# Kernel optimization log

Hardware: AMD Instinct MI355X
Metric: run time of the kernel (lower is better)

Reference implementation:

```python
import jax, jax.numpy as jnp
import numpy as np

WS = 8      # window size
NH = 8      # num heads
DIM = 256
SHIFT = WS // 2  # shift=True path


def _relative_position_index(ws):
    coords = np.stack(np.meshgrid(np.arange(ws), np.arange(ws), indexing='ij'))  # [2,ws,ws]
    cf = coords.reshape(2, -1)
    rel = cf[:, :, None] - cf[:, None, :]            # [2,ws*ws,ws*ws]
    rel = rel.transpose(1, 2, 0)
    rel[:, :, 0] += ws - 1
    rel[:, :, 1] += ws - 1
    rel[:, :, 0] *= 2 * ws - 1
    return rel.sum(-1).astype(np.int32)              # [ws*ws,ws*ws]


def setup_inputs() -> dict:
    key = jax.random.key(0)
    ks = jax.random.split(key, 7)
    B, H, W, C = 2, 256, 256, DIM
    x = jax.random.normal(ks[0], (B, H, W, C), dtype=jnp.float32)
    qkv_w = jax.random.normal(ks[1], (3 * C, C), dtype=jnp.float32) * 0.02
    qkv_b = jnp.zeros((3 * C,), dtype=jnp.float32)
    proj_w = jax.random.normal(ks[2], (C, C), dtype=jnp.float32) * 0.02
    proj_b = jnp.zeros((C,), dtype=jnp.float32)
    bias_table = jax.random.normal(ks[3], ((2 * WS - 1) ** 2, NH), dtype=jnp.float32) * 0.02
    rel_index = jnp.asarray(_relative_position_index(WS))
    return {"x": x, "qkv_w": qkv_w, "qkv_b": qkv_b, "proj_w": proj_w,
            "proj_b": proj_b, "bias_table": bias_table, "rel_index": rel_index}


def reference(x, qkv_w, qkv_b, proj_w, proj_b, bias_table, rel_index):
    B, H, W, C = x.shape
    ws, nh = WS, NH
    hd = C // nh
    scale = hd ** -0.5
    n = ws * ws
    # cyclic shift
    x = jnp.roll(x, shift=(-SHIFT, -SHIFT), axis=(1, 2))
    # window partition -> [B*nW, ws*ws, C]
    xw = x.reshape(B, H // ws, ws, W // ws, ws, C)
    xw = xw.transpose(0, 1, 3, 2, 4, 5).reshape(-1, n, C)
    # qkv projection (torch Linear: y = x @ W.T + b)
    qkv = xw @ qkv_w.T + qkv_b
    qkv = qkv.reshape(-1, n, 3, nh, hd).transpose(2, 0, 3, 1, 4)  # [3, nW, nh, n, hd]
    q, k, v = qkv[0] * scale, qkv[1], qkv[2]
    attn = jnp.einsum('whid,whjd->whij', q, k)  # [nW, nh, n, n]
    bias = bias_table[rel_index.reshape(-1)].reshape(n, n, nh).transpose(2, 0, 1)
    attn = jax.nn.softmax(attn + bias[None], axis=-1)
    out = jnp.einsum('whij,whjd->whid', attn, v)               # [nW, nh, n, hd]
    out = out.transpose(0, 2, 1, 3).reshape(-1, n, C)
    out = out @ proj_w.T + proj_b
    # window reverse
    out = out.reshape(B, H // ws, W // ws, ws, ws, C)
    out = out.transpose(0, 1, 3, 2, 4, 5).reshape(B, H, W, C)
    return jnp.roll(out, shift=(SHIFT, SHIFT), axis=(1, 2))
```

## Files before the change

kernel.cpp:

```cpp
#include <hip/hip_runtime.h>
#include <hip/hip_bf16.h>

typedef _Float16 f16;
typedef _Float16 f16x8 __attribute__((ext_vector_type(8)));
typedef _Float16 f16x4 __attribute__((ext_vector_type(4)));
typedef float f32x4 __attribute__((ext_vector_type(4)));

#define SCALE 0.17677669529663687f

#define QW_OFF   0
#define PW_OFF   393216
#define QB_OFF   524288
#define BF_OFF   527360

__global__ __launch_bounds__(256) void prep_kernel(
    const float* __restrict__ qkv_w, const float* __restrict__ qkv_b,
    const float* __restrict__ proj_w, const float* __restrict__ bias_table,
    const int* __restrict__ rel_index,
    f16* __restrict__ qw_h, f16* __restrict__ pw_h,
    float* __restrict__ qb_s, float* __restrict__ bias_fr) {
  int i = blockIdx.x * 256 + threadIdx.x;
  if (i < 768 * 256) {
    float s = (i < 256 * 256) ? SCALE : 1.0f;
    qw_h[i] = (f16)(qkv_w[i] * s);
  }
  if (i < 768) qb_s[i] = qkv_b[i] * (i < 256 ? SCALE : 1.0f);
  if (i < 256 * 256) pw_h[i] = (f16)proj_w[i];
  if (i < 8 * 4 * 4 * 256) {
    int h = i >> 12, rest = i & 4095;
    int qt = rest >> 10, kt = (rest >> 8) & 3, l = (rest >> 2) & 63, r = i & 3;
    int q = qt * 16 + (l & 15);
    int ke = kt * 16 + 4 * (l >> 4) + r;
    bias_fr[i] = bias_table[rel_index[q * 64 + ke] * 8 + h];
  }
}

__global__ __launch_bounds__(256, 2) void fused_kernel(
    const float* __restrict__ x, const f16* __restrict__ qw_h,
    const float* __restrict__ qb_s, const float* __restrict__ bias_fr,
    const f16* __restrict__ pw_h, const float* __restrict__ proj_b,
    float* __restrict__ out) {

  __shared__ f16 sx[64 * 264];
  __shared__ f16 stg[4][5120];

  const int tid = threadIdx.x;
  const int lane = tid & 63;
  const int wv = tid >> 6;
  const int lo = lane & 15, hi = lane >> 4;

  const int win = blockIdx.x;
  const int b = win >> 10, wh = (win >> 5) & 31, ww = win & 31;

  {
    const int t = tid >> 2, q4 = tid & 3;
    const int r = t >> 3, c = t & 7;
    const int gr = (wh * 8 + r + 4) & 255;
    const int gc = (ww * 8 + c + 4) & 255;
    const float* src = x + (((size_t)(b * 256 + gr)) * 256 + gc) * 256;
#pragma unroll
    for (int i = 0; i < 8; ++i) {
      const int off = q4 * 8 + i * 32;
      float4 v0 = *(const float4*)(src + off);
      float4 v1 = *(const float4*)(src + off + 4);
      f16x8 hv;
      hv[0] = (f16)v0.x; hv[1] = (f16)v0.y; hv[2] = (f16)v0.z; hv[3] = (f16)v0.w;
      hv[4] = (f16)v1.x; hv[5] = (f16)v1.y; hv[6] = (f16)v1.z; hv[7] = (f16)v1.w;
      *(f16x8*)&sx[t * 264 + off] = hv;
    }
  }
  __syncthreads();

  f16* ws_ = &stg[wv][0];
  f16x8 qf[2][4];
  f16x8 kf[2][4];
  f16x8 vf[2][2][2];

#pragma unroll
  for (int bn = 0; bn < 3; ++bn) {
    const int fwave = bn * 256 + wv * 64;

    f32x4 acc[4][4];
#pragma unroll
    for (int nt = 0; nt < 4; ++nt)
#pragma unroll
      for (int mt = 0; mt < 4; ++mt) acc[nt][mt] = (f32x4){0.f, 0.f, 0.f, 0.f};

    f16x8 bf[2][4];
#pragma unroll
    for (int nt = 0; nt < 4; ++nt)
      bf[0][nt] = *(const f16x8*)&qw_h[(size_t)(fwave + nt * 16 + lo) * 256 + 8 * hi];

#pragma unroll
    for (int kt = 0; kt < 8; ++kt) {
      const int cur = kt & 1;
      if (kt < 7) {
#pragma unroll
        for (int nt = 0; nt < 4; ++nt)
          bf[cur ^ 1][nt] = *(const f16x8*)&qw_h[(size_t)(fwave + nt * 16 + lo) * 256 + (kt + 1) * 32 + 8 * hi];
      }
      f16x8 a[4];
#pragma unroll
      for (int mt = 0; mt < 4; ++mt)
        a[mt] = *(const f16x8*)&sx[(mt * 16 + lo) * 264 + kt * 32 + 8 * hi];
#pragma unroll
      for (int nt = 0; nt < 4; ++nt)
#pragma unroll
        for (int mt = 0; mt < 4; ++mt) {
          if (bn < 2)
            acc[nt][mt] = __builtin_amdgcn_mfma_f32_16x16x32_f16(bf[cur][nt], a[mt], acc[nt][mt], 0, 0, 0);
          else
            acc[nt][mt] = __builtin_amdgcn_mfma_f32_16x16x32_f16(a[mt], bf[cur][nt], acc[nt][mt], 0, 0, 0);
        }
    }

    if (bn < 2) {
#pragma unroll
      for (int nt = 0; nt < 4; ++nt) {
        const f32x4 bias4 = *(const f32x4*)&qb_s[fwave + nt * 16 + 4 * hi];
        const int base = (nt >> 1) * 2560 + (nt & 1) * 16 + 4 * hi;
#pragma unroll
        for (int mt = 0; mt < 4; ++mt) {
          f16x4 t;
#pragma unroll
          for (int r4 = 0; r4 < 4; ++r4) t[r4] = (f16)(acc[nt][mt][r4] + bias4[r4]);
          *(f16x4*)&ws_[base + (mt * 16 + lo) * 40] = t;
        }
      }
#pragma unroll
      for (int hsel = 0; hsel < 2; ++hsel)
#pragma unroll
        for (int t4 = 0; t4 < 4; ++t4) {
          f16x8 fr = *(const f16x8*)&ws_[hsel * 2560 + (t4 * 16 + lo) * 40 + 8 * hi];
          if (bn == 0) qf[hsel][t4] = fr; else kf[hsel][t4] = fr;
        }
    } else {
#pragma unroll
      for (int nt = 0; nt < 4; ++nt) {
        const float bias = qb_s[fwave + nt * 16 + lo];
        const int row = (nt >> 1) * 32 + (nt & 1) * 16 + lo;
#pragma unroll
        for (int mt = 0; mt < 4; ++mt) {
          f16x4 t;
#pragma unroll
          for (int r4 = 0; r4 < 4; ++r4) t[r4] = (f16)(acc[nt][mt][r4] + bias);
          *(f16x4*)&ws_[row * 72 + mt * 16 + 4 * hi] = t;
        }
      }
#pragma unroll
      for (int hsel = 0; hsel < 2; ++hsel)
#pragma unroll
        for (int kk = 0; kk < 2; ++kk)
#pragma unroll
          for (int dt = 0; dt < 2; ++dt)
            vf[hsel][kk][dt] = *(const f16x8*)&ws_[(hsel * 32 + dt * 16 + lo) * 72 + kk * 32 + 8 * hi];
    }
  }

  __syncthreads();
  f16* sao = sx;
  const f32x4 zero = {0.f, 0.f, 0.f, 0.f};
  f16x8 vone;
#pragma unroll
  for (int j = 0; j < 8; ++j) vone[j] = (f16)1.0f;

#pragma unroll
  for (int hsel = 0; hsel < 2; ++hsel) {
    const int h = 2 * wv + hsel;
#pragma unroll
    for (int qh = 0; qh < 2; ++qh) {
      f32x4 s[2][4];
#pragma unroll
      for (int q2 = 0; q2 < 2; ++q2)
#pragma unroll
        for (int kt = 0; kt < 4; ++kt)
          s[q2][kt] = *(const f32x4*)&bias_fr[(((h * 4 + qh * 2 + q2) * 4 + kt) << 8) + lane * 4];
#pragma unroll
      for (int q2 = 0; q2 < 2; ++q2)
#pragma unroll
        for (int kt = 0; kt < 4; ++kt)
          s[q2][kt] = __builtin_amdgcn_mfma_f32_16x16x32_f16(kf[hsel][kt], qf[hsel][qh * 2 + q2], s[q2][kt], 0, 0, 0);

#pragma unroll
      for (int q2 = 0; q2 < 2; ++q2)
#pragma unroll
        for (int kt = 0; kt < 4; ++kt) {
          f16x4 t;
#pragma unroll
          for (int r4 = 0; r4 < 4; ++r4) t[r4] = (f16)__expf(s[q2][kt][r4]);
          *(f16x4*)&ws_[(q2 * 16 + lo) * 72 + kt * 16 + 4 * hi] = t;
        }

      f32x4 o[2][2], oa[2];
#pragma unroll
      for (int q2 = 0; q2 < 2; ++q2) {
        oa[q2] = zero;
#pragma unroll
        for (int dt = 0; dt < 2; ++dt) o[q2][dt] = zero;
      }
#pragma unroll
      for (int kk = 0; kk < 2; ++kk) {
        f16x8 pB[2];
#pragma unroll
        for (int q2 = 0; q2 < 2; ++q2)
          pB[q2] = *(const f16x8*)&ws_[(q2 * 16 + lo) * 72 + kk * 32 + 8 * hi];
#pragma unroll
        for (int q2 = 0; q2 < 2; ++q2) {
          oa[q2] = __builtin_amdgcn_mfma_f32_16x16x32_f16(vone, pB[q2], oa[q2], 0, 0, 0);
#pragma unroll
          for (int dt = 0; dt < 2; ++dt)
            o[q2][dt] = __builtin_amdgcn_mfma_f32_16x16x32_f16(vf[hsel][kk][dt], pB[q2], o[q2][dt], 0, 0, 0);
        }
      }

#pragma unroll
      for (int q2 = 0; q2 < 2; ++q2) {
        const float inv = __builtin_amdgcn_rcpf(oa[q2][0]);
        const int tok = qh * 32 + q2 * 16 + lo;
#pragma unroll
        for (int dt = 0; dt < 2; ++dt) {
          f16x4 t;
#pragma unroll
          for (int r4 = 0; r4 < 4; ++r4) t[r4] = (f16)(o[q2][dt][r4] * inv);
          *(f16x4*)&sao[tok * 264 + h * 32 + dt * 16 + 4 * hi] = t;
        }
      }
    }
  }

  __syncthreads();

  f32x4 acc[4][4];
#pragma unroll
  for (int j = 0; j < 4; ++j)
#pragma unroll
    for (int mt = 0; mt < 4; ++mt) acc[j][mt] = (f32x4){0.f, 0.f, 0.f, 0.f};

#pragma unroll
  for (int kt = 0; kt < 8; ++kt) {
    f16x8 a[4];
#pragma unroll
    for (int mt = 0; mt < 4; ++mt)
      a[mt] = *(const f16x8*)&sao[(mt * 16 + lo) * 264 + kt * 32 + 8 * hi];
#pragma unroll
    for (int j = 0; j < 4; ++j) {
      const int n = (4 * wv + j) * 16 + lo;
      f16x8 bfp = *(const f16x8*)&pw_h[(size_t)n * 256 + kt * 32 + 8 * hi];
#pragma unroll
      for (int mt = 0; mt < 4; ++mt)
        acc[j][mt] = __builtin_amdgcn_mfma_f32_16x16x32_f16(a[mt], bfp, acc[j][mt], 0, 0, 0);
    }
  }

#pragma unroll
  for (int j = 0; j < 4; ++j) {
    const int n = (4 * wv + j) * 16 + lo;
    const float pb = proj_b[n];
#pragma unroll
    for (int mt = 0; mt < 4; ++mt)
#pragma unroll
      for (int r4 = 0; r4 < 4; ++r4) {
        const int token = mt * 16 + 4 * hi + r4;
        const int tr = token >> 3, tc = token & 7;
        const int gr = (wh * 8 + tr + 4) & 255;
        const int gc = (ww * 8 + tc + 4) & 255;
        out[(((size_t)(b * 256 + gr)) * 256 + gc) * 256 + n] = acc[j][mt][r4] + pb;
      }
  }
}

extern "C" void kernel_launch(void* const* d_in, const int* in_sizes, int n_in,
                              void* d_out, int out_size, void* d_ws, size_t ws_size,
                              hipStream_t stream) {
  const float* x          = (const float*)d_in[0];
  const float* qkv_w      = (const float*)d_in[1];
  const float* qkv_b      = (const float*)d_in[2];
  const float* proj_w     = (const float*)d_in[3];
  const float* proj_b     = (const float*)d_in[4];
  const float* bias_table = (const float*)d_in[5];
  const int*   rel_index  = (const int*)d_in[6];
  float* out = (float*)d_out;

  char* ws = (char*)d_ws;
  f16*   qw_h    = (f16*)(ws + QW_OFF);
  f16*   pw_h    = (f16*)(ws + PW_OFF);
  float* qb_s    = (float*)(ws + QB_OFF);
  float* bias_fr = (float*)(ws + BF_OFF);

  prep_kernel<<<768, 256, 0, stream>>>(qkv_w, qkv_b, proj_w, bias_table, rel_index,
                                       qw_h, pw_h, qb_s, bias_fr);
  fused_kernel<<<2048, 256, 0, stream>>>(x, qw_h, qb_s, bias_fr, pw_h, proj_b, out);
}
```

Measured before the change: 166.6 us.

## Shrink LDS with XOR swizzle, split QKV by head, prefetch proj weights

Replaces the padded 264-stride shared tile with an XOR-swizzled 256-stride layout and shrinks the per-wave staging buffer by processing the QKV projection one head (32 features) at a time. The smaller LDS footprint together with launch_bounds raised to 3 blocks per CU aims for higher occupancy. The output projection now double-buffers its weight fragments from global memory so loads can overlap the MFMAs. The trade-off is that the 3-block bound caps registers per thread, which may cause spills, and the QKV loop now runs as more, smaller passes.

```diff
diff --git a/kernel.cpp b/kernel.cpp
--- a/kernel.cpp
+++ b/kernel.cpp
@@ -12,6 +12,8 @@
 #define PW_OFF   393216
 #define QB_OFF   524288
 #define BF_OFF   527360
+
+#define SW(row, col) (((row) << 8) + ((col) ^ (((row) & 7) << 3)))
 
 __global__ __launch_bounds__(256) void prep_kernel(
     const float* __restrict__ qkv_w, const float* __restrict__ qkv_b,
@@ -35,14 +37,14 @@
   }
 }
 
-__global__ __launch_bounds__(256, 2) void fused_kernel(
+__global__ __launch_bounds__(256, 3) void fused_kernel(
     const float* __restrict__ x, const f16* __restrict__ qw_h,
     const float* __restrict__ qb_s, const float* __restrict__ bias_fr,
     const f16* __restrict__ pw_h, const float* __restrict__ proj_b,
     float* __restrict__ out) {
 
-  __shared__ f16 sx[64 * 264];
-  __shared__ f16 stg[4][5120];
+  __shared__ f16 sx[64 * 256];
+  __shared__ f16 stg[4][2304];
 
   const int tid = threadIdx.x;
   const int lane = tid & 63;
@@ -66,7 +68,7 @@
       f16x8 hv;
       hv[0] = (f16)v0.x; hv[1] = (f16)v0.y; hv[2] = (f16)v0.z; hv[3] = (f16)v0.w;
       hv[4] = (f16)v1.x; hv[5] = (f16)v1.y; hv[6] = (f16)v1.z; hv[7] = (f16)v1.w;
-      *(f16x8*)&sx[t * 264 + off] = hv;
+      *(f16x8*)&sx[SW(t, off)] = hv;
     }
   }
   __syncthreads();
@@ -78,82 +80,84 @@
 
 #pragma unroll
   for (int bn = 0; bn < 3; ++bn) {
-    const int fwave = bn * 256 + wv * 64;
-
-    f32x4 acc[4][4];
-#pragma unroll
-    for (int nt = 0; nt < 4; ++nt)
-#pragma unroll
-      for (int mt = 0; mt < 4; ++mt) acc[nt][mt] = (f32x4){0.f, 0.f, 0.f, 0.f};
-
-    f16x8 bf[2][4];
-#pragma unroll
-    for (int nt = 0; nt < 4; ++nt)
-      bf[0][nt] = *(const f16x8*)&qw_h[(size_t)(fwave + nt * 16 + lo) * 256 + 8 * hi];
-
-#pragma unroll
-    for (int kt = 0; kt < 8; ++kt) {
-      const int cur = kt & 1;
-      if (kt < 7) {
-#pragma unroll
-        for (int nt = 0; nt < 4; ++nt)
-          bf[cur ^ 1][nt] = *(const f16x8*)&qw_h[(size_t)(fwave + nt * 16 + lo) * 256 + (kt + 1) * 32 + 8 * hi];
-      }
-      f16x8 a[4];
-#pragma unroll
-      for (int mt = 0; mt < 4; ++mt)
-        a[mt] = *(const f16x8*)&sx[(mt * 16 + lo) * 264 + kt * 32 + 8 * hi];
-#pragma unroll
-      for (int nt = 0; nt < 4; ++nt)
-#pragma unroll
-        for (int mt = 0; mt < 4; ++mt) {
-          if (bn < 2)
-            acc[nt][mt] = __builtin_amdgcn_mfma_f32_16x16x32_f16(bf[cur][nt], a[mt], acc[nt][mt], 0, 0, 0);
-          else
-            acc[nt][mt] = __builtin_amdgcn_mfma_f32_16x16x32_f16(a[mt], bf[cur][nt], acc[nt][mt], 0, 0, 0);
-        }
-    }
-
-    if (bn < 2) {
-#pragma unroll
-      for (int nt = 0; nt < 4; ++nt) {
-        const f32x4 bias4 = *(const f32x4*)&qb_s[fwave + nt * 16 + 4 * hi];
-        const int base = (nt >> 1) * 2560 + (nt & 1) * 16 + 4 * hi;
-#pragma unroll
-        for (int mt = 0; mt < 4; ++mt) {
-          f16x4 t;
-#pragma unroll
-          for (int r4 = 0; r4 < 4; ++r4) t[r4] = (f16)(acc[nt][mt][r4] + bias4[r4]);
-          *(f16x4*)&ws_[base + (mt * 16 + lo) * 40] = t;
-        }
-      }
-#pragma unroll
-      for (int hsel = 0; hsel < 2; ++hsel)
-#pragma unroll
-        for (int t4 = 0; t4 < 4; ++t4) {
-          f16x8 fr = *(const f16x8*)&ws_[hsel * 2560 + (t4 * 16 + lo) * 40 + 8 * hi];
-          if (bn == 0) qf[hsel][t4] = fr; else kf[hsel][t4] = fr;
-        }
-    } else {
-#pragma unroll
-      for (int nt = 0; nt < 4; ++nt) {
-        const float bias = qb_s[fwave + nt * 16 + lo];
-        const int row = (nt >> 1) * 32 + (nt & 1) * 16 + lo;
-#pragma unroll
-        for (int mt = 0; mt < 4; ++mt) {
-          f16x4 t;
-#pragma unroll
-          for (int r4 = 0; r4 < 4; ++r4) t[r4] = (f16)(acc[nt][mt][r4] + bias);
-          *(f16x4*)&ws_[row * 72 + mt * 16 + 4 * hi] = t;
-        }
-      }
-#pragma unroll
-      for (int hsel = 0; hsel < 2; ++hsel)
+#pragma unroll
+    for (int hsel = 0; hsel < 2; ++hsel) {
+      const int f0 = bn * 256 + wv * 64 + hsel * 32;
+
+      f32x4 acc[2][4];
+#pragma unroll
+      for (int n2 = 0; n2 < 2; ++n2)
+#pragma unroll
+        for (int mt = 0; mt < 4; ++mt) acc[n2][mt] = (f32x4){0.f, 0.f, 0.f, 0.f};
+
+      f16x8 bf[2][2];
+#pragma unroll
+      for (int n2 = 0; n2 < 2; ++n2)
+        bf[0][n2] = *(const f16x8*)&qw_h[(size_t)(f0 + n2 * 16 + lo) * 256 + 8 * hi];
+
+#pragma unroll
+      for (int kt = 0; kt < 8; ++kt) {
+        const int cur = kt & 1;
+        if (kt < 7) {
+#pragma unroll
+          for (int n2 = 0; n2 < 2; ++n2)
+            bf[cur ^ 1][n2] = *(const f16x8*)&qw_h[(size_t)(f0 + n2 * 16 + lo) * 256 + (kt + 1) * 32 + 8 * hi];
+        }
+        f16x8 a[4];
+#pragma unroll
+        for (int mt = 0; mt < 4; ++mt)
+          a[mt] = *(const f16x8*)&sx[SW(mt * 16 + lo, kt * 32 + 8 * hi)];
+#pragma unroll
+        for (int n2 = 0; n2 < 2; ++n2)
+#pragma unroll
+          for (int mt = 0; mt < 4; ++mt) {
+            if (bn < 2)
+              acc[n2][mt] = __builtin_amdgcn_mfma_f32_16x16x32_f16(bf[cur][n2], a[mt], acc[n2][mt], 0, 0, 0);
+            else
+              acc[n2][mt] = __builtin_amdgcn_mfma_f32_16x16x32_f16(a[mt], bf[cur][n2], acc[n2][mt], 0, 0, 0);
+          }
+      }
+
+      if (bn < 2) {
+#pragma unroll
+        for (int h2 = 0; h2 < 2; ++h2) {
+#pragma unroll
+          for (int n2 = 0; n2 < 2; ++n2) {
+            const f32x4 bias4 = *(const f32x4*)&qb_s[f0 + n2 * 16 + 4 * hi];
+#pragma unroll
+            for (int mtl = 0; mtl < 2; ++mtl) {
+              const int mt = h2 * 2 + mtl;
+              f16x4 t;
+#pragma unroll
+              for (int r4 = 0; r4 < 4; ++r4) t[r4] = (f16)(acc[n2][mt][r4] + bias4[r4]);
+              *(f16x4*)&ws_[(mtl * 16 + lo) * 40 + n2 * 16 + 4 * hi] = t;
+            }
+          }
+#pragma unroll
+          for (int t4l = 0; t4l < 2; ++t4l) {
+            f16x8 fr = *(const f16x8*)&ws_[(t4l * 16 + lo) * 40 + 8 * hi];
+            if (bn == 0) qf[hsel][h2 * 2 + t4l] = fr;
+            else         kf[hsel][h2 * 2 + t4l] = fr;
+          }
+        }
+      } else {
+#pragma unroll
+        for (int n2 = 0; n2 < 2; ++n2) {
+          const float bias = qb_s[f0 + n2 * 16 + lo];
+#pragma unroll
+          for (int mt = 0; mt < 4; ++mt) {
+            f16x4 t;
+#pragma unroll
+            for (int r4 = 0; r4 < 4; ++r4) t[r4] = (f16)(acc[n2][mt][r4] + bias);
+            *(f16x4*)&ws_[(n2 * 16 + lo) * 72 + mt * 16 + 4 * hi] = t;
+          }
+        }
 #pragma unroll
         for (int kk = 0; kk < 2; ++kk)
 #pragma unroll
           for (int dt = 0; dt < 2; ++dt)
-            vf[hsel][kk][dt] = *(const f16x8*)&ws_[(hsel * 32 + dt * 16 + lo) * 72 + kk * 32 + 8 * hi];
+            vf[hsel][kk][dt] = *(const f16x8*)&ws_[(dt * 16 + lo) * 72 + kk * 32 + 8 * hi];
+      }
     }
   }
 
@@ -222,7 +226,7 @@
           f16x4 t;
 #pragma unroll
           for (int r4 = 0; r4 < 4; ++r4) t[r4] = (f16)(o[q2][dt][r4] * inv);
-          *(f16x4*)&sao[tok * 264 + h * 32 + dt * 16 + 4 * hi] = t;
+          *(f16x4*)&sao[SW(tok, h * 32 + dt * 16 + 4 * hi)] = t;
         }
       }
     }
@@ -236,20 +240,28 @@
 #pragma unroll
     for (int mt = 0; mt < 4; ++mt) acc[j][mt] = (f32x4){0.f, 0.f, 0.f, 0.f};
 
+  f16x8 bfp[2][4];
+#pragma unroll
+  for (int j = 0; j < 4; ++j)
+    bfp[0][j] = *(const f16x8*)&pw_h[(size_t)((4 * wv + j) * 16 + lo) * 256 + 8 * hi];
+
 #pragma unroll
   for (int kt = 0; kt < 8; ++kt) {
+    const int cur = kt & 1;
+    if (kt < 7) {
+#pragma unroll
+      for (int j = 0; j < 4; ++j)
+        bfp[cur ^ 1][j] = *(const f16x8*)&pw_h[(size_t)((4 * wv + j) * 16 + lo) * 256 + (kt + 1) * 32 + 8 * hi];
+    }
     f16x8 a[4];
 #pragma unroll
     for (int mt = 0; mt < 4; ++mt)
-      a[mt] = *(const f16x8*)&sao[(mt * 16 + lo) * 264 + kt * 32 + 8 * hi];
-#pragma unroll
-    for (int j = 0; j < 4; ++j) {
-      const int n = (4 * wv + j) * 16 + lo;
-      f16x8 bfp = *(const f16x8*)&pw_h[(size_t)n * 256 + kt * 32 + 8 * hi];
+      a[mt] = *(const f16x8*)&sao[SW(mt * 16 + lo, kt * 32 + 8 * hi)];
+#pragma unroll
+    for (int j = 0; j < 4; ++j)
 #pragma unroll
       for (int mt = 0; mt < 4; ++mt)
-        acc[j][mt] = __builtin_amdgcn_mfma_f32_16x16x32_f16(a[mt], bfp, acc[j][mt], 0, 0, 0);
-    }
+        acc[j][mt] = __builtin_amdgcn_mfma_f32_16x16x32_f16(a[mt], bfp[cur][j], acc[j][mt], 0, 0, 0);
   }
 
 #pragma unroll
```

Measured after the change: 187.9 us. 12.8% more time.
